# Kernel optimization log

Hardware: AMD Instinct MI355X
Metric: run time of the kernel (lower is better)

Reference implementation:

```python
import jax, jax.numpy as jnp
import numpy as np

HIDDEN = 128
HEADS = 4
S = 128          # number of scenes
N = 64           # pedestrians per scene
TOTAL = S * N


def setup_inputs() -> dict:
    key = jax.random.key(0)
    ks = jax.random.split(key, 12)
    h = HIDDEN
    return {
        "node_features": jax.random.normal(ks[0], (TOTAL, h), jnp.float32),
        "positions": jax.random.normal(ks[1], (TOTAL, 2), jnp.float32),
        # rel_pos_encoder: Linear(2, h//2) -> ReLU -> Linear(h//2, h)
        "W1": jax.random.normal(ks[2], (h // 2, 2), jnp.float32) * 0.5,
        "b1": jax.random.normal(ks[3], (h // 2,), jnp.float32) * 0.02,
        "W2": jax.random.normal(ks[4], (h, h // 2), jnp.float32) * (1.0 / np.sqrt(h // 2)),
        "b2": jax.random.normal(ks[5], (h,), jnp.float32) * 0.02,
        # MultiheadAttention packed in-projection (q,k,v stacked) and out-projection
        "in_proj_w": jax.random.normal(ks[6], (3 * h, h), jnp.float32) * (1.0 / np.sqrt(h)),
        "in_proj_b": jax.random.normal(ks[7], (3 * h,), jnp.float32) * 0.02,
        "out_w": jax.random.normal(ks[8], (h, h), jnp.float32) * (1.0 / np.sqrt(h)),
        "out_b": jax.random.normal(ks[9], (h,), jnp.float32) * 0.02,
        # output_proj: Linear(2h, h)
        "proj_w": jax.random.normal(ks[10], (h, 2 * h), jnp.float32) * (1.0 / np.sqrt(2 * h)),
        "proj_b": jax.random.normal(ks[11], (h,), jnp.float32) * 0.02,
        "num_scenes": S,
        "peds_per_scene": N,
    }


def reference(node_features, positions, W1, b1, W2, b2,
              in_proj_w, in_proj_b, out_w, out_b, proj_w, proj_b,
              num_scenes, peds_per_scene):
    h = node_features.shape[-1]
    heads = HEADS
    dh = h // heads
    s, n = num_scenes, peds_per_scene

    feats = node_features.reshape(s, n, h)          # (S, n, h)
    pos = positions.reshape(s, n, 2)                # (S, n, 2)

    # rel[s, i, j] = pos[j] - pos[i]  (matches unsqueeze(0) - unsqueeze(1))
    rel = pos[:, None, :, :] - pos[:, :, None, :]   # (S, n, n, 2)
    rel_enc = jnp.maximum(rel @ W1.T + b1, 0.0) @ W2.T + b2  # (S, n, n, h)

    Wq, Wk, Wv = jnp.split(in_proj_w, 3, axis=0)
    bq, bk, bv = jnp.split(in_proj_b, 3, axis=0)

    # query: each ped i attends over keys j = feats[j] + rel_enc[i, j]
    key_in = feats[:, None, :, :] + rel_enc          # (S, n, n, h)
    q = (feats @ Wq.T + bq).reshape(s, n, heads, dh)             # (S, n, H, dh)
    k = (key_in @ Wk.T + bk).reshape(s, n, n, heads, dh)         # (S, n, n, H, dh)
    v = (key_in @ Wv.T + bv).reshape(s, n, n, heads, dh)

    scores = jnp.einsum('sihd,sijhd->shij', q, k) / np.sqrt(dh)  # (S, H, n, n)
    attn = jax.nn.softmax(scores, axis=-1)
    ctx = jnp.einsum('shij,sijhd->sihd', attn, v).reshape(s, n, h)
    attn_out = ctx @ out_w.T + out_b                              # (S, n, h)

    combined = jnp.concatenate([feats, attn_out], axis=-1)       # (S, n, 2h)
    out = combined @ proj_w.T + proj_b                            # (S, n, h)
    return out.reshape(s * n, h)
```

## Files before the change

### kernel.cpp

```cpp
#include <hip/hip_runtime.h>
#include <hip/hip_bf16.h>


typedef unsigned int u32;
#define SCALE 0.17677669529663689f

__device__ __forceinline__ float bl(u32 u){ union{u32 x; float f;} c; c.x = u << 16; return c.f; }
__device__ __forceinline__ float bh(u32 u){ union{u32 x; float f;} c; c.x = u & 0xffff0000u; return c.f; }
__device__ __forceinline__ u32 pk(float a, float b){
  union{float f; u32 x;} ca, cb; ca.f = a; cb.f = b;
  u32 ua = (ca.x + 0x7fffu + ((ca.x >> 16) & 1u)) >> 16;
  u32 ub = (cb.x + 0x7fffu + ((cb.x >> 16) & 1u)) >> 16;
  return ua | (ub << 16);
}
__device__ __forceinline__ float dot8(uint4 u, float4 f0, float4 f1, float acc){
  acc = fmaf(bl(u.x), f0.x, acc); acc = fmaf(bh(u.x), f0.y, acc);
  acc = fmaf(bl(u.y), f0.z, acc); acc = fmaf(bh(u.y), f0.w, acc);
  acc = fmaf(bl(u.z), f1.x, acc); acc = fmaf(bh(u.z), f1.y, acc);
  acc = fmaf(bl(u.w), f1.z, acc); acc = fmaf(bh(u.w), f1.w, acc);
  return acc;
}
__device__ __forceinline__ void wsync(){
  __builtin_amdgcn_s_waitcnt(0xC07F);
  __builtin_amdgcn_wave_barrier();
}

__global__ __launch_bounds__(256, 2) void ee_setup(
    const float* __restrict__ nf, const float* __restrict__ b2,
    const float* __restrict__ ipw, const float* __restrict__ ipb,
    const float* __restrict__ w2,
    const float* __restrict__ ow, const float* __restrict__ pw,
    float* __restrict__ W2KT, float* __restrict__ W2VT,
    u32* __restrict__ WQB, u32* __restrict__ OWB, u32* __restrict__ PWB,
    u32* __restrict__ KBt, u32* __restrict__ VB)
{
  const int tid = threadIdx.x, b = blockIdx.x;
  const int cg = tid >> 6, l = tid & 63;
  const float2* ipw2 = (const float2*)ipw;
  const float2* ow2  = (const float2*)ow;
  const float2* pw2  = (const float2*)pw;

  if (b >= 544) {
    for (int k = 0; k < 16; ++k) {
      int i = (b - 544) * 4096 + k * 256 + tid;
      if (i < 8192)       { float2 f = ipw2[i];        WQB[i]        = pk(f.x, f.y); }
      else if (i < 16384) { float2 f = ow2[i - 8192];  OWB[i - 8192] = pk(f.x, f.y); }
      else                { float2 f = pw2[i - 16384]; PWB[i - 16384]= pk(f.x, f.y); }
    }
    return;
  }
  if (b >= 512) {
    int t = (b - 512) * 4 + cg;
    int kv = t & 1, e = t >> 1;
    int c0 = 2 * l;
    const float4* rp = (const float4*)ipw + (size_t)(128 + kv * 128 + c0) * 32;
    const float* w2e = w2 + __builtin_amdgcn_readfirstlane(e);
    float a0 = 0.f, a1 = 0.f;
    #pragma unroll 8
    for (int c4 = 0; c4 < 32; ++c4) {
      float4 wa = rp[c4], wb = rp[32 + c4];
      float x0 = w2e[(4 * c4 + 0) * 64];
      float x1 = w2e[(4 * c4 + 1) * 64];
      float x2 = w2e[(4 * c4 + 2) * 64];
      float x3 = w2e[(4 * c4 + 3) * 64];
      a0 = fmaf(wa.x, x0, a0); a0 = fmaf(wa.y, x1, a0);
      a0 = fmaf(wa.z, x2, a0); a0 = fmaf(wa.w, x3, a0);
      a1 = fmaf(wb.x, x0, a1); a1 = fmaf(wb.y, x1, a1);
      a1 = fmaf(wb.z, x2, a1); a1 = fmaf(wb.w, x3, a1);
    }
    float* dst = kv ? W2VT : W2KT;
    ((float2*)dst)[e * 64 + l] = make_float2(a0, a1);
    return;
  }

  const int s = b >> 2, kv = (b >> 1) & 1, hlf = b & 1;
  __shared__ __align__(16) u32 fbS[64][68];
  __shared__ u32 vtS[64][33];
  const float2* nf2 = (const float2*)nf;
  const float2* b22 = (const float2*)b2;

  for (int idx = tid; idx < 4096; idx += 256) {
    int j = idx >> 6, mw = idx & 63;
    float2 f = nf2[((s << 6) + j) * 64 + mw];
    float2 bb = b22[mw];
    fbS[j][mw] = pk(f.x + bb.x, f.y + bb.y);
  }
  __syncthreads();

  uint4 fr[16];
  {
    const uint4* frow = (const uint4*)&fbS[l][0];
    #pragma unroll
    for (int k = 0; k < 16; ++k) fr[k] = frow[k];
  }
  #pragma unroll 1
  for (int p = 0; p < 8; ++p) {
    int c0 = hlf * 64 + cg * 16 + 2 * p;
    int r0 = 128 + kv * 128 + c0;
    const float4* w0 = (const float4*)ipw +
                       (size_t)__builtin_amdgcn_readfirstlane(r0) * 32;
    const float4* w1r = w0 + 32;
    float a0 = ipb[r0], a1 = ipb[r0 + 1];
    #pragma unroll
    for (int k = 0; k < 16; ++k) {
      uint4 F = fr[k];
      float4 wa = w0[2 * k],  wb = w0[2 * k + 1];
      float4 xa = w1r[2 * k], xb = w1r[2 * k + 1];
      float e0 = bl(F.x), e1 = bh(F.x), e2 = bl(F.y), e3 = bh(F.y);
      float e4 = bl(F.z), e5 = bh(F.z), e6 = bl(F.w), e7 = bh(F.w);
      a0 = fmaf(e0, wa.x, a0); a0 = fmaf(e1, wa.y, a0);
      a0 = fmaf(e2, wa.z, a0); a0 = fmaf(e3, wa.w, a0);
      a0 = fmaf(e4, wb.x, a0); a0 = fmaf(e5, wb.y, a0);
      a0 = fmaf(e6, wb.z, a0); a0 = fmaf(e7, wb.w, a0);
      a1 = fmaf(e0, xa.x, a1); a1 = fmaf(e1, xa.y, a1);
      a1 = fmaf(e2, xa.z, a1); a1 = fmaf(e3, xa.w, a1);
      a1 = fmaf(e4, xb.x, a1); a1 = fmaf(e5, xb.y, a1);
      a1 = fmaf(e6, xb.z, a1); a1 = fmaf(e7, xb.w, a1);
    }
    u32 v = pk(a0, a1);
    int cw = hlf * 32 + cg * 8 + p;
    if (kv == 0) KBt[(((s << 6) + cw) << 6) + l] = v;
    else         vtS[l][cg * 8 + p] = v;
  }
  if (kv == 1) {
    __syncthreads();
    int r = tid >> 2, cb = (tid & 3) * 8;
    #pragma unroll
    for (int k = 0; k < 8; ++k)
      VB[(((s << 6) + r) << 6) + hlf * 32 + cb + k] = vtS[r][cb + k];
  }
}

__global__ __launch_bounds__(256, 2) void ee_main(
    const float* __restrict__ nf, const float* __restrict__ pos,
    const float* __restrict__ w1, const float* __restrict__ b1,
    const float* __restrict__ ipb,
    const float* __restrict__ ob, const float* __restrict__ pb,
    const float* __restrict__ W2KT, const float* __restrict__ W2VT,
    const u32* __restrict__ WQB, const u32* __restrict__ OWB,
    const u32* __restrict__ PWB,
    const u32* __restrict__ KBt, const u32* __restrict__ VB,
    float* __restrict__ outp)
{
  __shared__ __align__(16) float pxS[64], pyS[64], w1xS[64], w1yS[64], b1S[64];
  __shared__ __align__(16) float fqS[4][4][132];
  __shared__ __align__(16) float qS [4][4][132];
  __shared__ __align__(16) float qwS[4][4][4][68];
  __shared__ __align__(16) float atS[4][4][4][68];
  __shared__ __align__(16) float whS[4][4][4][68];

  const int tid = threadIdx.x;
  const int s = blockIdx.x >> 2, qt = blockIdx.x & 3;
  const int w = tid >> 6, l = tid & 63;
  const int c0 = 2 * l;

  if (tid < 64) {
    float2 p = ((const float2*)pos)[(s << 6) + tid];
    pxS[tid] = p.x; pyS[tid] = p.y;
    float2 wv = ((const float2*)w1)[tid];
    w1xS[tid] = wv.x; w1yS[tid] = wv.y;
    b1S[tid] = b1[tid];
  }
  __syncthreads();

  int il[4], ig[4];
  #pragma unroll
  for (int t = 0; t < 4; ++t) { il[t] = qt * 16 + 4 * w + t; ig[t] = (s << 6) + il[t]; }

  #pragma unroll
  for (int t = 0; t < 4; ++t)
    *(float2*)&fqS[w][t][c0] = ((const float2*)nf)[ig[t] * 64 + l];
  wsync();

  {
    float2 bq = ((const float2*)ipb)[l];
    float a0[4], a1[4];
    #pragma unroll
    for (int t = 0; t < 4; ++t) { a0[t] = bq.x; a1[t] = bq.y; }
    const uint4* W4 = (const uint4*)WQB;
    #pragma unroll 4
    for (int m8 = 0; m8 < 16; ++m8) {
      uint4 ua = W4[c0 * 16 + m8];
      uint4 ub = W4[(c0 + 1) * 16 + m8];
      #pragma unroll
      for (int t = 0; t < 4; ++t) {
        float4 f0 = *(const float4*)&fqS[w][t][8 * m8];
        float4 f1 = *(const float4*)&fqS[w][t][8 * m8 + 4];
        a0[t] = dot8(ua, f0, f1, a0[t]);
        a1[t] = dot8(ub, f0, f1, a1[t]);
      }
    }
    #pragma unroll
    for (int t = 0; t < 4; ++t)
      *(float2*)&qS[w][t][c0] = make_float2(a0[t], a1[t]);
  }
  wsync();

  {
    const float4* G4 = (const float4*)W2KT;
    #pragma unroll
    for (int hd = 0; hd < 4; ++hd) {
      float acc[4] = {0.f, 0.f, 0.f, 0.f};
      #pragma unroll
      for (int dq = 0; dq < 8; ++dq) {
        float4 g = G4[l * 32 + hd * 8 + dq];
        #pragma unroll
        for (int t = 0; t < 4; ++t) {
          float4 qf = *(const float4*)&qS[w][t][hd * 32 + 4 * dq];
          acc[t] = fmaf(g.x, qf.x, acc[t]); acc[t] = fmaf(g.y, qf.y, acc[t]);
          acc[t] = fmaf(g.z, qf.z, acc[t]); acc[t] = fmaf(g.w, qf.w, acc[t]);
        }
      }
      #pragma unroll
      for (int t = 0; t < 4; ++t) qwS[w][t][hd][l] = acc[t];
    }
  }
  wsync();

  float at[4][4];
  float pix[4], piy[4];
  {
    float pjx = pxS[l], pjy = pyS[l];
    float rx[4], ry[4];
    #pragma unroll
    for (int t = 0; t < 4; ++t) {
      pix[t] = pxS[il[t]]; piy[t] = pyS[il[t]];
      rx[t] = pjx - pix[t]; ry[t] = pjy - piy[t];
    }
    float sc[4][4];
    #pragma unroll
    for (int t = 0; t < 4; ++t)
      #pragma unroll
      for (int hd = 0; hd < 4; ++hd) sc[t][hd] = 0.f;

    const u32* kbp = KBt + (s << 12);
    #pragma unroll 8
    for (int m2 = 0; m2 < 32; ++m2) {
      u32 u0 = kbp[((2 * m2) << 6) + l];
      u32 u1 = kbp[((2 * m2 + 1) << 6) + l];
      const int hd = m2 >> 3;
      #pragma unroll
      for (int t = 0; t < 4; ++t) {
        float4 qf = *(const float4*)&qS[w][t][4 * m2];
        sc[t][hd] = fmaf(bl(u0), qf.x, sc[t][hd]);
        sc[t][hd] = fmaf(bh(u0), qf.y, sc[t][hd]);
        sc[t][hd] = fmaf(bl(u1), qf.z, sc[t][hd]);
        sc[t][hd] = fmaf(bh(u1), qf.w, sc[t][hd]);
      }
    }
    #pragma unroll 2
    for (int eb = 0; eb < 8; ++eb) {
      float4 wx0 = *(const float4*)&w1xS[8 * eb];
      float4 wx1 = *(const float4*)&w1xS[8 * eb + 4];
      float4 wy0 = *(const float4*)&w1yS[8 * eb];
      float4 wy1 = *(const float4*)&w1yS[8 * eb + 4];
      float4 bb0 = *(const float4*)&b1S[8 * eb];
      float4 bb1 = *(const float4*)&b1S[8 * eb + 4];
      #pragma unroll
      for (int t = 0; t < 4; ++t) {
        float h0 = fmaxf(0.f, fmaf(rx[t], wx0.x, fmaf(ry[t], wy0.x, bb0.x)));
        float h1 = fmaxf(0.f, fmaf(rx[t], wx0.y, fmaf(ry[t], wy0.y, bb0.y)));
        float h2 = fmaxf(0.f, fmaf(rx[t], wx0.z, fmaf(ry[t], wy0.z, bb0.z)));
        float h3 = fmaxf(0.f, fmaf(rx[t], wx0.w, fmaf(ry[t], wy0.w, bb0.w)));
        float h4 = fmaxf(0.f, fmaf(rx[t], wx1.x, fmaf(ry[t], wy1.x, bb1.x)));
        float h5 = fmaxf(0.f, fmaf(rx[t], wx1.y, fmaf(ry[t], wy1.y, bb1.y)));
        float h6 = fmaxf(0.f, fmaf(rx[t], wx1.z, fmaf(ry[t], wy1.z, bb1.z)));
        float h7 = fmaxf(0.f, fmaf(rx[t], wx1.w, fmaf(ry[t], wy1.w, bb1.w)));
        #pragma unroll
        for (int hd = 0; hd < 4; ++hd) {
          float4 q0 = *(const float4*)&qwS[w][t][hd][8 * eb];
          float4 q1 = *(const float4*)&qwS[w][t][hd][8 * eb + 4];
          float a = sc[t][hd];
          a = fmaf(q0.x, h0, a); a = fmaf(q0.y, h1, a);
          a = fmaf(q0.z, h2, a); a = fmaf(q0.w, h3, a);
          a = fmaf(q1.x, h4, a); a = fmaf(q1.y, h5, a);
          a = fmaf(q1.z, h6, a); a = fmaf(q1.w, h7, a);
          sc[t][hd] = a;
        }
      }
    }
    #pragma unroll
    for (int t = 0; t < 4; ++t) {
      #pragma unroll
      for (int hd = 0; hd < 4; ++hd) {
        float v = sc[t][hd] * SCALE;
        float m = v;
        #pragma unroll
        for (int off = 32; off > 0; off >>= 1) m = fmaxf(m, __shfl_xor(m, off));
        float p = __expf(v - m);
        float su = p;
        #pragma unroll
        for (int off = 32; off > 0; off >>= 1) su += __shfl_xor(su, off);
#if __has_builtin(__builtin_amdgcn_rcpf)
        at[t][hd] = p * __builtin_amdgcn_rcpf(su);
#else
        at[t][hd] = p / su;
#endif
        atS[w][t][hd][l] = at[t][hd];
      }
    }
  }
  wsync();

  {
    float wx = w1xS[l], wy = w1yS[l], bb = b1S[l];
    float wh[4][4];
    #pragma unroll
    for (int t = 0; t < 4; ++t)
      #pragma unroll
      for (int hd = 0; hd < 4; ++hd) wh[t][hd] = 0.f;
    #pragma unroll 4
    for (int j4 = 0; j4 < 16; ++j4) {
      float4 px = *(const float4*)&pxS[4 * j4];
      float4 py = *(const float4*)&pyS[4 * j4];
      #pragma unroll
      for (int t = 0; t < 4; ++t) {
        float4 a0v = *(const float4*)&atS[w][t][0][4 * j4];
        float4 a1v = *(const float4*)&atS[w][t][1][4 * j4];
        float4 a2v = *(const float4*)&atS[w][t][2][4 * j4];
        float4 a3v = *(const float4*)&atS[w][t][3][4 * j4];
        float h;
        h = fmaxf(0.f, fmaf(px.x - pix[t], wx, fmaf(py.x - piy[t], wy, bb)));
        wh[t][0] = fmaf(a0v.x, h, wh[t][0]); wh[t][1] = fmaf(a1v.x, h, wh[t][1]);
        wh[t][2] = fmaf(a2v.x, h, wh[t][2]); wh[t][3] = fmaf(a3v.x, h, wh[t][3]);
        h = fmaxf(0.f, fmaf(px.y - pix[t], wx, fmaf(py.y - piy[t], wy, bb)));
        wh[t][0] = fmaf(a0v.y, h, wh[t][0]); wh[t][1] = fmaf(a1v.y, h, wh[t][1]);
        wh[t][2] = fmaf(a2v.y, h, wh[t][2]); wh[t][3] = fmaf(a3v.y, h, wh[t][3]);
        h = fmaxf(0.f, fmaf(px.z - pix[t], wx, fmaf(py.z - piy[t], wy, bb)));
        wh[t][0] = fmaf(a0v.z, h, wh[t][0]); wh[t][1] = fmaf(a1v.z, h, wh[t][1]);
        wh[t][2] = fmaf(a2v.z, h, wh[t][2]); wh[t][3] = fmaf(a3v.z, h, wh[t][3]);
        h = fmaxf(0.f, fmaf(px.w - pix[t], wx, fmaf(py.w - piy[t], wy, bb)));
        wh[t][0] = fmaf(a0v.w, h, wh[t][0]); wh[t][1] = fmaf(a1v.w, h, wh[t][1]);
        wh[t][2] = fmaf(a2v.w, h, wh[t][2]); wh[t][3] = fmaf(a3v.w, h, wh[t][3]);
      }
    }
    #pragma unroll
    for (int t = 0; t < 4; ++t)
      #pragma unroll
      for (int hd = 0; hd < 4; ++hd) whS[w][t][hd][l] = wh[t][hd];
  }
  wsync();

  {
    const int hd = l >> 4;
    float cx0[4] = {0,0,0,0}, cx1[4] = {0,0,0,0};
    const float2* V2 = (const float2*)W2VT;
    const u32* vbp = VB + (s << 12);
    #pragma unroll 4
    for (int n4 = 0; n4 < 16; ++n4) {
      float2 g0 = V2[((4 * n4 + 0) << 6) + l];
      float2 g1 = V2[((4 * n4 + 1) << 6) + l];
      float2 g2 = V2[((4 * n4 + 2) << 6) + l];
      float2 g3 = V2[((4 * n4 + 3) << 6) + l];
      u32 v0 = vbp[((4 * n4 + 0) << 6) + l];
      u32 v1 = vbp[((4 * n4 + 1) << 6) + l];
      u32 v2 = vbp[((4 * n4 + 2) << 6) + l];
      u32 v3 = vbp[((4 * n4 + 3) << 6) + l];
      #pragma unroll
      for (int t = 0; t < 4; ++t) {
        float4 whv = *(const float4*)&whS[w][t][hd][4 * n4];
        float4 atv = *(const float4*)&atS[w][t][hd][4 * n4];
        float a0 = cx0[t], a1 = cx1[t];
        a0 = fmaf(whv.x, g0.x, a0); a1 = fmaf(whv.x, g0.y, a1);
        a0 = fmaf(atv.x, bl(v0), a0); a1 = fmaf(atv.x, bh(v0), a1);
        a0 = fmaf(whv.y, g1.x, a0); a1 = fmaf(whv.y, g1.y, a1);
        a0 = fmaf(atv.y, bl(v1), a0); a1 = fmaf(atv.y, bh(v1), a1);
        a0 = fmaf(whv.z, g2.x, a0); a1 = fmaf(whv.z, g2.y, a1);
        a0 = fmaf(atv.z, bl(v2), a0); a1 = fmaf(atv.z, bh(v2), a1);
        a0 = fmaf(whv.w, g3.x, a0); a1 = fmaf(whv.w, g3.y, a1);
        a0 = fmaf(atv.w, bl(v3), a0); a1 = fmaf(atv.w, bh(v3), a1);
        cx0[t] = a0; cx1[t] = a1;
      }
    }
    wsync();
    #pragma unroll
    for (int t = 0; t < 4; ++t)
      *(float2*)&qS[w][t][c0] = make_float2(cx0[t], cx1[t]);
  }
  wsync();

  {
    float2 b = ((const float2*)ob)[l];
    float a0[4], a1[4];
    #pragma unroll
    for (int t = 0; t < 4; ++t) { a0[t] = b.x; a1[t] = b.y; }
    const uint4* W4 = (const uint4*)OWB;
    #pragma unroll 4
    for (int m8 = 0; m8 < 16; ++m8) {
      uint4 ua = W4[c0 * 16 + m8];
      uint4 ub = W4[(c0 + 1) * 16 + m8];
      #pragma unroll
      for (int t = 0; t < 4; ++t) {
        float4 f0 = *(const float4*)&qS[w][t][8 * m8];
        float4 f1 = *(const float4*)&qS[w][t][8 * m8 + 4];
        a0[t] = dot8(ua, f0, f1, a0[t]);
        a1[t] = dot8(ub, f0, f1, a1[t]);
      }
    }
    wsync();
    #pragma unroll
    for (int t = 0; t < 4; ++t)
      *(float2*)(&whS[w][t][0][0] + c0) = make_float2(a0[t], a1[t]);
  }
  wsync();

  {
    float2 b = ((const float2*)pb)[l];
    float a0[4], a1[4];
    #pragma unroll
    for (int t = 0; t < 4; ++t) { a0[t] = b.x; a1[t] = b.y; }
    const uint4* W4 = (const uint4*)PWB;
    #pragma unroll 2
    for (int m8 = 0; m8 < 16; ++m8) {
      uint4 ua = W4[c0 * 32 + m8];
      uint4 ub = W4[(c0 + 1) * 32 + m8];
      uint4 uc = W4[c0 * 32 + 16 + m8];
      uint4 ud = W4[(c0 + 1) * 32 + 16 + m8];
      #pragma unroll
      for (int t = 0; t < 4; ++t) {
        float4 f0 = *(const float4*)&fqS[w][t][8 * m8];
        float4 f1 = *(const float4*)&fqS[w][t][8 * m8 + 4];
        float4 g0 = *(const float4*)(&whS[w][t][0][0] + 8 * m8);
        float4 g1 = *(const float4*)(&whS[w][t][0][0] + 8 * m8 + 4);
        a0[t] = dot8(ua, f0, f1, a0[t]);
        a1[t] = dot8(ub, f0, f1, a1[t]);
        a0[t] = dot8(uc, g0, g1, a0[t]);
        a1[t] = dot8(ud, g0, g1, a1[t]);
      }
    }
    #pragma unroll
    for (int t = 0; t < 4; ++t)
      ((float2*)outp)[ig[t] * 64 + l] = make_float2(a0[t], a1[t]);
  }
}

extern "C" void kernel_launch(void* const* d_in, const int* in_sizes, int n_in,
                              void* d_out, int out_size, void* d_ws, size_t ws_size,
                              hipStream_t stream) {
  (void)in_sizes; (void)n_in; (void)out_size; (void)ws_size;
  const float* nf  = (const float*)d_in[0];
  const float* pos = (const float*)d_in[1];
  const float* w1  = (const float*)d_in[2];
  const float* b1  = (const float*)d_in[3];
  const float* w2  = (const float*)d_in[4];
  const float* b2  = (const float*)d_in[5];
  const float* ipw = (const float*)d_in[6];
  const float* ipb = (const float*)d_in[7];
  const float* ow  = (const float*)d_in[8];
  const float* ob  = (const float*)d_in[9];
  const float* pw  = (const float*)d_in[10];
  const float* pb  = (const float*)d_in[11];

  char* ws = (char*)d_ws;
  float* W2KT = (float*)(ws);
  float* W2VT = (float*)(ws + (32 << 10));
  u32* WQB  = (u32*)(ws + (64 << 10));
  u32* OWB  = (u32*)(ws + (96 << 10));
  u32* PWB  = (u32*)(ws + (128 << 10));
  u32* KBt  = (u32*)(ws + (192 << 10));
  u32* VB   = (u32*)(ws + (192 << 10) + (128 * 4096 * 4));

  ee_setup<<<dim3(552), dim3(256), 0, stream>>>(nf, b2, ipw, ipb, w2, ow, pw,
                                                W2KT, W2VT, WQB, OWB, PWB, KBt, VB);
  ee_main<<<dim3(512), dim3(256), 0, stream>>>(nf, pos, w1, b1, ipb, ob, pb,
                                               W2KT, W2VT, WQB, OWB, PWB,
                                               KBt, VB, (float*)d_out);
}
```

Baseline: 172.9 us.

## Halve queries per block, double grid, read fp32 weights directly

The main kernel now handles 2 query rows per wave instead of 4 and launches 1024 blocks instead of 512, with shared buffers shrunk to match. The launch bound is raised to 4 blocks per CU. The setup kernel no longer converts the Q, out-proj and output-proj weights to bf16; the main kernel reads the fp32 weights directly. This removes setup blocks and bf16 unpacking and adds parallelism and occupancy, at the cost of twice the per-block weight traffic per query and more pressure on the register budget.

```diff
diff --git a/kernel.cpp b/kernel.cpp
--- a/kernel.cpp
+++ b/kernel.cpp
@@ -13,11 +13,11 @@
   u32 ub = (cb.x + 0x7fffu + ((cb.x >> 16) & 1u)) >> 16;
   return ua | (ub << 16);
 }
-__device__ __forceinline__ float dot8(uint4 u, float4 f0, float4 f1, float acc){
-  acc = fmaf(bl(u.x), f0.x, acc); acc = fmaf(bh(u.x), f0.y, acc);
-  acc = fmaf(bl(u.y), f0.z, acc); acc = fmaf(bh(u.y), f0.w, acc);
-  acc = fmaf(bl(u.z), f1.x, acc); acc = fmaf(bh(u.z), f1.y, acc);
-  acc = fmaf(bl(u.w), f1.z, acc); acc = fmaf(bh(u.w), f1.w, acc);
+__device__ __forceinline__ float dot8f(float4 w0, float4 w1, float4 f0, float4 f1, float acc){
+  acc = fmaf(w0.x, f0.x, acc); acc = fmaf(w0.y, f0.y, acc);
+  acc = fmaf(w0.z, f0.z, acc); acc = fmaf(w0.w, f0.w, acc);
+  acc = fmaf(w1.x, f1.x, acc); acc = fmaf(w1.y, f1.y, acc);
+  acc = fmaf(w1.z, f1.z, acc); acc = fmaf(w1.w, f1.w, acc);
   return acc;
 }
 __device__ __forceinline__ void wsync(){
@@ -29,26 +29,12 @@
     const float* __restrict__ nf, const float* __restrict__ b2,
     const float* __restrict__ ipw, const float* __restrict__ ipb,
     const float* __restrict__ w2,
-    const float* __restrict__ ow, const float* __restrict__ pw,
     float* __restrict__ W2KT, float* __restrict__ W2VT,
-    u32* __restrict__ WQB, u32* __restrict__ OWB, u32* __restrict__ PWB,
     u32* __restrict__ KBt, u32* __restrict__ VB)
 {
   const int tid = threadIdx.x, b = blockIdx.x;
   const int cg = tid >> 6, l = tid & 63;
-  const float2* ipw2 = (const float2*)ipw;
-  const float2* ow2  = (const float2*)ow;
-  const float2* pw2  = (const float2*)pw;
-
-  if (b >= 544) {
-    for (int k = 0; k < 16; ++k) {
-      int i = (b - 544) * 4096 + k * 256 + tid;
-      if (i < 8192)       { float2 f = ipw2[i];        WQB[i]        = pk(f.x, f.y); }
-      else if (i < 16384) { float2 f = ow2[i - 8192];  OWB[i - 8192] = pk(f.x, f.y); }
-      else                { float2 f = pw2[i - 16384]; PWB[i - 16384]= pk(f.x, f.y); }
-    }
-    return;
-  }
+
   if (b >= 512) {
     int t = (b - 512) * 4 + cg;
     int kv = t & 1, e = t >> 1;
@@ -131,26 +117,25 @@
   }
 }
 
-__global__ __launch_bounds__(256, 2) void ee_main(
+__global__ __launch_bounds__(256, 4) void ee_main(
     const float* __restrict__ nf, const float* __restrict__ pos,
     const float* __restrict__ w1, const float* __restrict__ b1,
-    const float* __restrict__ ipb,
-    const float* __restrict__ ob, const float* __restrict__ pb,
+    const float* __restrict__ ipw, const float* __restrict__ ipb,
+    const float* __restrict__ ow, const float* __restrict__ ob,
+    const float* __restrict__ pw, const float* __restrict__ pb,
     const float* __restrict__ W2KT, const float* __restrict__ W2VT,
-    const u32* __restrict__ WQB, const u32* __restrict__ OWB,
-    const u32* __restrict__ PWB,
     const u32* __restrict__ KBt, const u32* __restrict__ VB,
     float* __restrict__ outp)
 {
   __shared__ __align__(16) float pxS[64], pyS[64], w1xS[64], w1yS[64], b1S[64];
-  __shared__ __align__(16) float fqS[4][4][132];
-  __shared__ __align__(16) float qS [4][4][132];
-  __shared__ __align__(16) float qwS[4][4][4][68];
-  __shared__ __align__(16) float atS[4][4][4][68];
-  __shared__ __align__(16) float whS[4][4][4][68];
+  __shared__ __align__(16) float fqS[4][2][132];
+  __shared__ __align__(16) float qS [4][2][132];
+  __shared__ __align__(16) float qwS[4][2][4][68];
+  __shared__ __align__(16) float atS[4][2][4][68];
+  __shared__ __align__(16) float whS[4][2][4][68];
 
   const int tid = threadIdx.x;
-  const int s = blockIdx.x >> 2, qt = blockIdx.x & 3;
+  const int s = blockIdx.x >> 3, qt = blockIdx.x & 7;
   const int w = tid >> 6, l = tid & 63;
   const int c0 = 2 * l;
 
@@ -163,35 +148,34 @@
   }
   __syncthreads();
 
-  int il[4], ig[4];
+  int il[2], ig[2];
   #pragma unroll
-  for (int t = 0; t < 4; ++t) { il[t] = qt * 16 + 4 * w + t; ig[t] = (s << 6) + il[t]; }
+  for (int t = 0; t < 2; ++t) { il[t] = qt * 8 + 2 * w + t; ig[t] = (s << 6) + il[t]; }
 
   #pragma unroll
-  for (int t = 0; t < 4; ++t)
+  for (int t = 0; t < 2; ++t)
     *(float2*)&fqS[w][t][c0] = ((const float2*)nf)[ig[t] * 64 + l];
   wsync();
 
   {
     float2 bq = ((const float2*)ipb)[l];
-    float a0[4], a1[4];
-    #pragma unroll
-    for (int t = 0; t < 4; ++t) { a0[t] = bq.x; a1[t] = bq.y; }
-    const uint4* W4 = (const uint4*)WQB;
+    float a0[2] = {bq.x, bq.x}, a1[2] = {bq.y, bq.y};
+    const float4* Wa = (const float4*)ipw + (size_t)c0 * 32;
+    const float4* Wb = Wa + 32;
     #pragma unroll 4
     for (int m8 = 0; m8 < 16; ++m8) {
-      uint4 ua = W4[c0 * 16 + m8];
-      uint4 ub = W4[(c0 + 1) * 16 + m8];
-      #pragma unroll
-      for (int t = 0; t < 4; ++t) {
+      float4 wa0 = Wa[2 * m8], wa1 = Wa[2 * m8 + 1];
+      float4 wb0 = Wb[2 * m8], wb1 = Wb[2 * m8 + 1];
+      #pragma unroll
+      for (int t = 0; t < 2; ++t) {
         float4 f0 = *(const float4*)&fqS[w][t][8 * m8];
         float4 f1 = *(const float4*)&fqS[w][t][8 * m8 + 4];
-        a0[t] = dot8(ua, f0, f1, a0[t]);
-        a1[t] = dot8(ub, f0, f1, a1[t]);
-      }
-    }
-    #pragma unroll
-    for (int t = 0; t < 4; ++t)
+        a0[t] = dot8f(wa0, wa1, f0, f1, a0[t]);
+        a1[t] = dot8f(wb0, wb1, f0, f1, a1[t]);
+      }
+    }
+    #pragma unroll
+    for (int t = 0; t < 2; ++t)
       *(float2*)&qS[w][t][c0] = make_float2(a0[t], a1[t]);
   }
   wsync();
@@ -200,36 +184,36 @@
     const float4* G4 = (const float4*)W2KT;
     #pragma unroll
     for (int hd = 0; hd < 4; ++hd) {
-      float acc[4] = {0.f, 0.f, 0.f, 0.f};
+      float acc[2] = {0.f, 0.f};
       #pragma unroll
       for (int dq = 0; dq < 8; ++dq) {
         float4 g = G4[l * 32 + hd * 8 + dq];
         #pragma unroll
-        for (int t = 0; t < 4; ++t) {
+        for (int t = 0; t < 2; ++t) {
           float4 qf = *(const float4*)&qS[w][t][hd * 32 + 4 * dq];
           acc[t] = fmaf(g.x, qf.x, acc[t]); acc[t] = fmaf(g.y, qf.y, acc[t]);
           acc[t] = fmaf(g.z, qf.z, acc[t]); acc[t] = fmaf(g.w, qf.w, acc[t]);
         }
       }
       #pragma unroll
-      for (int t = 0; t < 4; ++t) qwS[w][t][hd][l] = acc[t];
-    }
-  }
-  wsync();
-
-  float at[4][4];
-  float pix[4], piy[4];
+      for (int t = 0; t < 2; ++t) qwS[w][t][hd][l] = acc[t];
+    }
+  }
+  wsync();
+
+  float at[2][4];
+  float pix[2], piy[2];
   {
     float pjx = pxS[l], pjy = pyS[l];
-    float rx[4], ry[4];
-    #pragma unroll
-    for (int t = 0; t < 4; ++t) {
+    float rx[2], ry[2];
+    #pragma unroll
+    for (int t = 0; t < 2; ++t) {
       pix[t] = pxS[il[t]]; piy[t] = pyS[il[t]];
       rx[t] = pjx - pix[t]; ry[t] = pjy - piy[t];
     }
-    float sc[4][4];
-    #pragma unroll
-    for (int t = 0; t < 4; ++t)
+    float sc[2][4];
+    #pragma unroll
+    for (int t = 0; t < 2; ++t)
       #pragma unroll
       for (int hd = 0; hd < 4; ++hd) sc[t][hd] = 0.f;
 
@@ -240,7 +224,7 @@
       u32 u1 = kbp[((2 * m2 + 1) << 6) + l];
       const int hd = m2 >> 3;
       #pragma unroll
-      for (int t = 0; t < 4; ++t) {
+      for (int t = 0; t < 2; ++t) {
         float4 qf = *(const float4*)&qS[w][t][4 * m2];
         sc[t][hd] = fmaf(bl(u0), qf.x, sc[t][hd]);
         sc[t][hd] = fmaf(bh(u0), qf.y, sc[t][hd]);
@@ -257,7 +241,7 @@
       float4 bb0 = *(const float4*)&b1S[8 * eb];
       float4 bb1 = *(const float4*)&b1S[8 * eb + 4];
       #pragma unroll
-      for (int t = 0; t < 4; ++t) {
+      for (int t = 0; t < 2; ++t) {
         float h0 = fmaxf(0.f, fmaf(rx[t], wx0.x, fmaf(ry[t], wy0.x, bb0.x)));
         float h1 = fmaxf(0.f, fmaf(rx[t], wx0.y, fmaf(ry[t], wy0.y, bb0.y)));
         float h2 = fmaxf(0.f, fmaf(rx[t], wx0.z, fmaf(ry[t], wy0.z, bb0.z)));
@@ -280,7 +264,7 @@
       }
     }
     #pragma unroll
-    for (int t = 0; t < 4; ++t) {
+    for (int t = 0; t < 2; ++t) {
       #pragma unroll
       for (int hd = 0; hd < 4; ++hd) {
         float v = sc[t][hd] * SCALE;
@@ -304,9 +288,9 @@
 
   {
     float wx = w1xS[l], wy = w1yS[l], bb = b1S[l];
-    float wh[4][4];
-    #pragma unroll
-    for (int t = 0; t < 4; ++t)
+    float wh[2][4];
+    #pragma unroll
+    for (int t = 0; t < 2; ++t)
       #pragma unroll
       for (int hd = 0; hd < 4; ++hd) wh[t][hd] = 0.f;
     #pragma unroll 4
@@ -314,7 +298,7 @@
       float4 px = *(const float4*)&pxS[4 * j4];
       float4 py = *(const float4*)&pyS[4 * j4];
       #pragma unroll
-      for (int t = 0; t < 4; ++t) {
+      for (int t = 0; t < 2; ++t) {
         float4 a0v = *(const float4*)&atS[w][t][0][4 * j4];
         float4 a1v = *(const float4*)&atS[w][t][1][4 * j4];
         float4 a2v = *(const float4*)&atS[w][t][2][4 * j4];
@@ -335,7 +319,7 @@
       }
     }
     #pragma unroll
-    for (int t = 0; t < 4; ++t)
+    for (int t = 0; t < 2; ++t)
       #pragma unroll
       for (int hd = 0; hd < 4; ++hd) whS[w][t][hd][l] = wh[t][hd];
   }
@@ -343,7 +327,7 @@
 
   {
     const int hd = l >> 4;
-    float cx0[4] = {0,0,0,0}, cx1[4] = {0,0,0,0};
+    float cx0[2] = {0, 0}, cx1[2] = {0, 0};
     const float2* V2 = (const float2*)W2VT;
     const u32* vbp = VB + (s << 12);
     #pragma unroll 4
@@ -357,7 +341,7 @@
       u32 v2 = vbp[((4 * n4 + 2) << 6) + l];
       u32 v3 = vbp[((4 * n4 + 3) << 6) + l];
       #pragma unroll
-      for (int t = 0; t < 4; ++t) {
+      for (int t = 0; t < 2; ++t) {
         float4 whv = *(const float4*)&whS[w][t][hd][4 * n4];
         float4 atv = *(const float4*)&atS[w][t][hd][4 * n4];
         float a0 = cx0[t], a1 = cx1[t];
@@ -374,62 +358,60 @@
     }
     wsync();
     #pragma unroll
-    for (int t = 0; t < 4; ++t)
+    for (int t = 0; t < 2; ++t)
       *(float2*)&qS[w][t][c0] = make_float2(cx0[t], cx1[t]);
   }
   wsync();
 
   {
     float2 b = ((const float2*)ob)[l];
-    float a0[4], a1[4];
-    #pragma unroll
-    for (int t = 0; t < 4; ++t) { a0[t] = b.x; a1[t] = b.y; }
-    const uint4* W4 = (const uint4*)OWB;
+    float a0[2] = {b.x, b.x}, a1[2] = {b.y, b.y};
+    const float4* Wa = (const float4*)ow + (size_t)c0 * 32;
+    const float4* Wb = Wa + 32;
     #pragma unroll 4
     for (int m8 = 0; m8 < 16; ++m8) {
-      uint4 ua = W4[c0 * 16 + m8];
-      uint4 ub = W4[(c0 + 1) * 16 + m8];
-      #pragma unroll
-      for (int t = 0; t < 4; ++t) {
+      float4 wa0 = Wa[2 * m8], wa1 = Wa[2 * m8 + 1];
+      float4 wb0 = Wb[2 * m8], wb1 = Wb[2 * m8 + 1];
+      #pragma unroll
+      for (int t = 0; t < 2; ++t) {
         float4 f0 = *(const float4*)&qS[w][t][8 * m8];
         float4 f1 = *(const float4*)&qS[w][t][8 * m8 + 4];
-        a0[t] = dot8(ua, f0, f1, a0[t]);
-        a1[t] = dot8(ub, f0, f1, a1[t]);
+        a0[t] = dot8f(wa0, wa1, f0, f1, a0[t]);
+        a1[t] = dot8f(wb0, wb1, f0, f1, a1[t]);
       }
     }
     wsync();
     #pragma unroll
-    for (int t = 0; t < 4; ++t)
+    for (int t = 0; t < 2; ++t)
       *(float2*)(&whS[w][t][0][0] + c0) = make_float2(a0[t], a1[t]);
   }
   wsync();
 
   {
     float2 b = ((const float2*)pb)[l];
-    float a0[4], a1[4];
-    #pragma unroll
-    for (int t = 0; t < 4; ++t) { a0[t] = b.x; a1[t] = b.y; }
-    const uint4* W4 = (const uint4*)PWB;
+    float a0[2] = {b.x, b.x}, a1[2] = {b.y, b.y};
+    const float4* Pa = (const float4*)pw + (size_t)c0 * 64;
+    const float4* Pb = Pa + 64;
     #pragma unroll 2
     for (int m8 = 0; m8 < 16; ++m8) {
-      uint4 ua = W4[c0 * 32 + m8];
-      uint4 ub = W4[(c0 + 1) * 32 + m8];
-      uint4 uc = W4[c0 * 32 + 16 + m8];
-      uint4 ud = W4[(c0 + 1) * 32 + 16 + m8];
-      #pragma unroll
-      for (int t = 0; t < 4; ++t) {
+      float4 pa0 = Pa[2 * m8],      pa1 = Pa[2 * m8 + 1];
+      float4 pa2 = Pa[32 + 2 * m8], pa3 = Pa[33 + 2 * m8];
+      float4 pb0 = Pb[2 * m8],      pb1 = Pb[2 * m8 + 1];
+      float4 pb2 = Pb[32 + 2 * m8], pb3 = Pb[33 + 2 * m8];
+      #pragma unroll
+      for (int t = 0; t < 2; ++t) {
         float4 f0 = *(const float4*)&fqS[w][t][8 * m8];
         float4 f1 = *(const float4*)&fqS[w][t][8 * m8 + 4];
         float4 g0 = *(const float4*)(&whS[w][t][0][0] + 8 * m8);
         float4 g1 = *(const float4*)(&whS[w][t][0][0] + 8 * m8 + 4);
-        a0[t] = dot8(ua, f0, f1, a0[t]);
-        a1[t] = dot8(ub, f0, f1, a1[t]);
-        a0[t] = dot8(uc, g0, g1, a0[t]);
-        a1[t] = dot8(ud, g0, g1, a1[t]);
-      }
-    }
-    #pragma unroll
-    for (int t = 0; t < 4; ++t)
+        a0[t] = dot8f(pa0, pa1, f0, f1, a0[t]);
+        a1[t] = dot8f(pb0, pb1, f0, f1, a1[t]);
+        a0[t] = dot8f(pa2, pa3, g0, g1, a0[t]);
+        a1[t] = dot8f(pb2, pb3, g0, g1, a1[t]);
+      }
+    }
+    #pragma unroll
+    for (int t = 0; t < 2; ++t)
       ((float2*)outp)[ig[t] * 64 + l] = make_float2(a0[t], a1[t]);
   }
 }
@@ -454,15 +436,12 @@
   char* ws = (char*)d_ws;
   float* W2KT = (float*)(ws);
   float* W2VT = (float*)(ws + (32 << 10));
-  u32* WQB  = (u32*)(ws + (64 << 10));
-  u32* OWB  = (u32*)(ws + (96 << 10));
-  u32* PWB  = (u32*)(ws + (128 << 10));
-  u32* KBt  = (u32*)(ws + (192 << 10));
-  u32* VB   = (u32*)(ws + (192 << 10) + (128 * 4096 * 4));
-
-  ee_setup<<<dim3(552), dim3(256), 0, stream>>>(nf, b2, ipw, ipb, w2, ow, pw,
-                                                W2KT, W2VT, WQB, OWB, PWB, KBt, VB);
-  ee_main<<<dim3(512), dim3(256), 0, stream>>>(nf, pos, w1, b1, ipb, ob, pb,
-                                               W2KT, W2VT, WQB, OWB, PWB,
-                                               KBt, VB, (float*)d_out);
-}
+  u32* KBt  = (u32*)(ws + (64 << 10));
+  u32* VB   = (u32*)(ws + (64 << 10) + (128 * 4096 * 4));
+
+  ee_setup<<<dim3(544), dim3(256), 0, stream>>>(nf, b2, ipw, ipb, w2,
+                                                W2KT, W2VT, KBt, VB);
+  ee_main<<<dim3(1024), dim3(256), 0, stream>>>(nf, pos, w1, b1, ipw, ipb,
+                                                ob ? ow : ow, ob, pw, pb,
+                                                W2KT, W2VT, KBt, VB, (float*)d_out);
+}
```

Result: slower. 253.1 us (+46.3%).
